# Kernel optimization log

Measured on AMD Instinct MI355X. Metric: run time of the kernel, lower is better.

## Reference

```python
import jax, jax.numpy as jnp
import numpy as np

N_NODES = 50000
N_EDGES = 800000
K = 15          # kernel points
P_DIM = 3
IN_DIM = 32
OUT_DIM = 64
KP_EXTENT = 0.6


def setup_inputs() -> dict:
    key = jax.random.key(0)
    k1, k2, k3, k4, k5, k6 = jax.random.split(key, 6)
    pos = jax.random.normal(k1, (N_NODES, P_DIM), dtype=jnp.float32)
    feat = jax.random.normal(k2, (N_NODES, IN_DIM), dtype=jnp.float32)
    # kernel point layout inside a ball of the given radius (load_kernels stand-in)
    kernel_points = jax.random.normal(k3, (K, P_DIM), dtype=jnp.float32) * 0.5
    kernel_points = kernel_points.at[0].set(0.0)  # fixed center point
    weights = jax.random.normal(k4, (K, IN_DIM, OUT_DIM), dtype=jnp.float32) * (1.0 / np.sqrt(IN_DIM))
    edge_src = jax.random.randint(k5, (N_EDGES,), 0, N_NODES, dtype=jnp.int32)
    edge_dst = jax.random.randint(k6, (N_EDGES,), 0, N_NODES, dtype=jnp.int32)
    return {"pos": pos, "feat": feat, "kernel_points": kernel_points,
            "weights": weights, "edge_src": edge_src, "edge_dst": edge_dst}


def reference(pos, feat, kernel_points, weights, edge_src, edge_dst):
    n_nodes = pos.shape[0]
    # per-edge relative position: src - dst  [E, p]
    y = pos[edge_src] - pos[edge_dst]
    # distance to each kernel point  [E, k]
    diff = y[:, None, :] - kernel_points[None, :, :]
    dist = jnp.sqrt(jnp.sum(diff * diff, axis=-1))
    # linear correlation influence  [E, k]
    m = jax.nn.relu(1.0 - dist / KP_EXTENT)
    # per-edge weighted features  [E, k, in]
    f = feat[edge_src]
    contrib = m[:, :, None] * f[:, None, :]
    # segment-reduce onto destination nodes  [N, k, in]
    weighted_f = jax.ops.segment_sum(contrib, edge_dst, num_segments=n_nodes)
    # per-kernel-point matmul and sum over kernel points  [N, out]
    return jnp.einsum('nki,kio->no', weighted_f, weights)
```

## Files before the change

### kernel.cpp

```cpp
#include <hip/hip_runtime.h>
#include <hip/hip_fp16.h>

#define N_NODES 50000
#define N_EDGES 800000
#define KPTS 15
#define IN_DIM 32
#define OUT_DIM 64
#define KP_EXTENT 0.6f
#define INV_EXT (1.0f / KP_EXTENT)
#define EXT2 (KP_EXTENT * KP_EXTENT)

#define CAP 131072
#define NREP 16
#define SEG_CAP (CAP / NREP)
#define CNT_STRIDE 32
#define K1_BLOCKS (N_EDGES / 256)
#define SUBB 8
#define WPS (SUBB * 4)

#define PCNT_OFF 32768
#define FEATH_OFF (1u << 20)
#define LIST_OFF  (8u << 20)
#define SLOT_OFF  (32u << 20)
#define SCAP_MAX 16

typedef unsigned int uint;
typedef _Float16 f16x8 __attribute__((ext_vector_type(8)));
typedef float f32x4 __attribute__((ext_vector_type(4)));

union FU { uint u[4]; f16x8 h; };

static __device__ __forceinline__ float h2f16(uint u) {
    return __half2float(__ushort_as_half((unsigned short)(u & 0xffffu)));
}
static __device__ __forceinline__ uint pack2(float lo, float hi) {
    return (uint)__half_as_ushort(__float2half_rn(lo))
         | ((uint)__half_as_ushort(__float2half_rn(hi)) << 16);
}

__global__ __launch_bounds__(256) void geom_compact(
    const float* __restrict__ pos,
    const float* __restrict__ feat,
    const float* __restrict__ kp,
    const int*   __restrict__ esrc,
    const int*   __restrict__ edst,
    int*         __restrict__ cnt,
    int*         __restrict__ pcnt,
    uint2*       __restrict__ lists,
    uint*        __restrict__ featH,
    float4*      __restrict__ outz,
    uint*        __restrict__ slots16,
    const int scap)
{
    __shared__ int s_wavecnt[KPTS][4];
    __shared__ int s_woff[KPTS][4];
    __shared__ int s_base[KPTS];

    const int tid  = threadIdx.x;
    const int wv   = tid >> 6;
    const int lane = tid & 63;
    const int rep  = blockIdx.x & (NREP - 1);

    const int e = blockIdx.x * 256 + tid;

    outz[e] = make_float4(0.0f, 0.0f, 0.0f, 0.0f);
    {
        const float2 fv = ((const float2*)feat)[e];
        featH[e] = pack2(fv.x, fv.y);
    }

    const int s = esrc[e];
    const int d = edst[e];

    const float yx = pos[s * 3 + 0] - pos[d * 3 + 0];
    const float yy = pos[s * 3 + 1] - pos[d * 3 + 1];
    const float yz = pos[s * 3 + 2] - pos[d * 3 + 2];

    float d2v[KPTS];
    unsigned act = 0;
    #pragma unroll
    for (int k = 0; k < KPTS; ++k) {
        const float dx = yx - kp[k * 3 + 0];
        const float dy = yy - kp[k * 3 + 1];
        const float dz = yz - kp[k * 3 + 2];
        const float d2 = dx * dx + dy * dy + dz * dz;
        d2v[k] = d2;
        if (d2 < EXT2) act |= (1u << k);
    }

    const int nact = __popc(act);
    int ti = 0;
    if (nact > 0) ti = atomicAdd(pcnt + d, nact);

    unsigned long long kmask[KPTS];
    #pragma unroll
    for (int k = 0; k < KPTS; ++k) {
        kmask[k] = __ballot((act >> k) & 1u);
        if (lane == 0) s_wavecnt[k][wv] = __popcll(kmask[k]);
    }
    __syncthreads();

    if (tid < KPTS) {
        int o0 = 0;
        #pragma unroll
        for (int w = 0; w < 4; ++w) {
            s_woff[tid][w] = o0;
            o0 += s_wavecnt[tid][w];
        }
        s_base[tid] = (o0 > 0)
            ? atomicAdd(&cnt[(tid * NREP + rep) * CNT_STRIDE], o0) : 0;
    }
    __syncthreads();

    const unsigned long long lt = (lane == 63) ? 0x7fffffffffffffffull
                                               : ((1ull << lane) - 1ull);
    #pragma unroll
    for (int k = 0; k < KPTS; ++k) {
        const unsigned long long mask = kmask[k];
        if (mask == 0ull) continue;
        if ((act >> k) & 1u) {
            const int rank = __popcll(mask & lt);
            const int idx  = s_base[k] + s_woff[k][wv] + rank;

            const int t = ti;
            ++ti;
            const unsigned ey = (t < scap)
                ? (unsigned)((d * scap + t) * OUT_DIM)
                : (0x80000000u | (unsigned)d);

            if (idx < SEG_CAP) {
                const float mk = 1.0f - sqrtf(d2v[k]) * INV_EXT;
                const unsigned mh =
                    (unsigned)__half_as_ushort(__float2half(mk));
                lists[(size_t)k * CAP + (size_t)rep * SEG_CAP + idx] =
                    make_uint2(((unsigned)s << 16) | mh, ey);
            } else if (!(ey & 0x80000000u)) {
                uint* row = slots16 + (ey >> 1);
                #pragma unroll
                for (int j = 0; j < OUT_DIM / 2; ++j) row[j] = 0u;
            }
        }
    }
}

__global__ __launch_bounds__(256) void pair_matmul(
    const uint*  __restrict__ featH,
    const float* __restrict__ W,
    const int*   __restrict__ cnt,
    const uint2* __restrict__ lists,
    float*       __restrict__ out,
    uint*        __restrict__ slots16)
{
    const int seg  = blockIdx.x % (KPTS * NREP);
    const int sub  = blockIdx.x / (KPTS * NREP);
    const int k    = seg >> 4;
    const int rep  = seg & (NREP - 1);
    const int wv   = threadIdx.x >> 6;
    const int lane = threadIdx.x & 63;
    const int col  = lane & 15;
    const int grp  = lane >> 4;

    uint bu[4][4];
    const float* __restrict__ Wk = W + k * (IN_DIM * OUT_DIM);
    #pragma unroll
    for (int t = 0; t < 4; ++t) {
        #pragma unroll
        for (int j = 0; j < 4; ++j) {
            const int kk = grp * 8 + 2 * j;
            const float wa = Wk[kk * OUT_DIM + t * 16 + col];
            const float wb = Wk[(kk + 1) * OUT_DIM + t * 16 + col];
            bu[t][j] = pack2(wa, wb);
        }
    }
    #pragma unroll
    for (int t = 0; t < 4; ++t)
        #pragma unroll
        for (int j = 0; j < 4; ++j)
            asm volatile("" : "+v"(bu[t][j]));

    int n = cnt[seg * CNT_STRIDE];
    if (n > SEG_CAP) n = SEG_CAP;
    const uint2* __restrict__ list =
        lists + (size_t)k * CAP + (size_t)rep * SEG_CAP;
    const int nsteps = (n + 15) >> 4;

    const int w = sub * 4 + wv;
    for (int s = w; s < nsteps; s += WPS) {
        const int pi = s * 16 + col;
        const uint2 ent = (pi < n) ? list[pi] : make_uint2(0u, 0xFFFFFFFFu);

        const uint src = ent.x >> 16;
        FU A;
        {
            const uint* __restrict__ fp = featH + src * 16 + grp * 4;
            #pragma unroll
            for (int j = 0; j < 4; ++j) A.u[j] = fp[j];
        }
        const float mym = h2f16(ent.x);

        f32x4 C0 = {0,0,0,0}, C1 = {0,0,0,0}, C2 = {0,0,0,0}, C3 = {0,0,0,0};
        {
            FU b0, b1, b2, b3;
            #pragma unroll
            for (int j = 0; j < 4; ++j) {
                b0.u[j] = bu[0][j]; b1.u[j] = bu[1][j];
                b2.u[j] = bu[2][j]; b3.u[j] = bu[3][j];
            }
            C0 = __builtin_amdgcn_mfma_f32_16x16x32_f16(A.h, b0.h, C0, 0, 0, 0);
            C1 = __builtin_amdgcn_mfma_f32_16x16x32_f16(A.h, b1.h, C1, 0, 0, 0);
            C2 = __builtin_amdgcn_mfma_f32_16x16x32_f16(A.h, b2.h, C2, 0, 0, 0);
            C3 = __builtin_amdgcn_mfma_f32_16x16x32_f16(A.h, b3.h, C3, 0, 0, 0);
        }

        #pragma unroll
        for (int i = 0; i < 4; ++i) {
            const int r = grp * 4 + i;
            const float mr = __shfl(mym, r);
            const uint  er = (uint)__shfl((int)ent.y, r);
            if (er == 0xFFFFFFFFu) continue;
            const float v0 = mr * C0[i];
            const float v1 = mr * C1[i];
            const float v2 = mr * C2[i];
            const float v3 = mr * C3[i];
            if (!(er & 0x80000000u)) {
                __half* __restrict__ sp = (__half*)slots16 + (size_t)er + col;
                sp[0]  = __float2half_rn(v0);
                sp[16] = __float2half_rn(v1);
                sp[32] = __float2half_rn(v2);
                sp[48] = __float2half_rn(v3);
            } else {
                float* __restrict__ op = out + (size_t)(er & 0xffffu) * OUT_DIM + col;
                atomicAdd(op +  0, v0);
                atomicAdd(op + 16, v1);
                atomicAdd(op + 32, v2);
                atomicAdd(op + 48, v3);
            }
        }
    }
}

__global__ __launch_bounds__(256) void node_reduce(
    const int*  __restrict__ pcnt,
    const uint* __restrict__ slots16,
    float*      __restrict__ out,
    const int scap)
{
    const int wv   = threadIdx.x >> 6;
    const int lane = threadIdx.x & 63;
    const int node = blockIdx.x * 8 + wv * 2 + (lane >> 5);
    const int l    = lane & 31;

    const int raw = pcnt[node];
    int deg = raw;
    if (deg > scap) deg = scap;

    const uint* __restrict__ sp =
        slots16 + (size_t)node * ((size_t)scap * 32) + l;

    float a0 = 0.0f, a1 = 0.0f, b0 = 0.0f, b1 = 0.0f;
    int j = 0;
    for (; j + 1 < deg; j += 2) {
        const uint u0 = sp[(size_t)j * 32];
        const uint u1 = sp[(size_t)(j + 1) * 32];
        a0 += h2f16(u0); a1 += h2f16(u0 >> 16);
        b0 += h2f16(u1); b1 += h2f16(u1 >> 16);
    }
    if (j < deg) {
        const uint u0 = sp[(size_t)j * 32];
        a0 += h2f16(u0); a1 += h2f16(u0 >> 16);
    }

    float o0 = a0 + b0;
    float o1 = a1 + b1;
    if (raw > scap) {
        const float2 prev = ((const float2*)out)[(size_t)node * 32 + l];
        o0 += prev.x; o1 += prev.y;
    }
    ((float2*)out)[(size_t)node * 32 + l] = make_float2(o0, o1);
}

extern "C" void kernel_launch(void* const* d_in, const int* in_sizes, int n_in,
                              void* d_out, int out_size, void* d_ws, size_t ws_size,
                              hipStream_t stream)
{
    const float* pos  = (const float*)d_in[0];
    const float* feat = (const float*)d_in[1];
    const float* kp   = (const float*)d_in[2];
    const float* W    = (const float*)d_in[3];
    const int* esrc   = (const int*)d_in[4];
    const int* edst   = (const int*)d_in[5];
    float* out        = (float*)d_out;

    int*   cnt     = (int*)d_ws;
    int*   pcnt    = (int*)((char*)d_ws + PCNT_OFF);
    uint*  featH   = (uint*)((char*)d_ws + FEATH_OFF);
    uint2* lists   = (uint2*)((char*)d_ws + LIST_OFF);
    uint*  slots16 = (uint*)((char*)d_ws + SLOT_OFF);

    const size_t layer_bytes = (size_t)N_NODES * OUT_DIM * 2;
    int scap = 0;
    if (ws_size >= (size_t)SLOT_OFF + layer_bytes) {
        scap = (int)((ws_size - (size_t)SLOT_OFF) / layer_bytes);
        if (scap > SCAP_MAX) scap = SCAP_MAX;
    }

    hipMemsetAsync(d_ws, 0, 262144, stream);

    geom_compact<<<K1_BLOCKS, 256, 0, stream>>>(pos, feat, kp, esrc, edst,
                                                cnt, pcnt, lists, featH,
                                                (float4*)out, slots16, scap);
    pair_matmul<<<SUBB * KPTS * NREP, 256, 0, stream>>>(featH, W, cnt, lists,
                                                        out, slots16);
    if (scap > 0)
        node_reduce<<<N_NODES / 8, 256, 0, stream>>>(pcnt, slots16, out, scap);
}
```

Before: 114.6 us.

## Prepack fp16 weights, prefetch next list entry, fold influence into MFMA input

The fp32-to-fp16 weight packing moves into the first kernel, which writes a packed WH buffer, so pair_matmul blocks load ready-made fp16 pairs instead of converting per block. The pair loop now software-pipelines the next list entry load, and the influence scalar is multiplied into the fp16 feature operand before the MFMA, removing per-row shuffles and multiplies. The number of sub-blocks per segment is halved, giving fewer, longer-running blocks. Scaling in fp16 before the matmul slightly changes rounding, and the smaller grid may reduce parallelism.

After: 113.8 us. Within noise of the previous version (-0.7%).

```diff
diff --git a/kernel.cpp b/kernel.cpp
--- a/kernel.cpp
+++ b/kernel.cpp
@@ -15,10 +15,11 @@
 #define SEG_CAP (CAP / NREP)
 #define CNT_STRIDE 32
 #define K1_BLOCKS (N_EDGES / 256)
-#define SUBB 8
+#define SUBB 4
 #define WPS (SUBB * 4)
 
 #define PCNT_OFF 32768
+#define WH_OFF   262144
 #define FEATH_OFF (1u << 20)
 #define LIST_OFF  (8u << 20)
 #define SLOT_OFF  (32u << 20)
@@ -29,6 +30,7 @@
 typedef float f32x4 __attribute__((ext_vector_type(4)));
 
 union FU { uint u[4]; f16x8 h; };
+union HU { unsigned short us; _Float16 h; };
 
 static __device__ __forceinline__ float h2f16(uint u) {
     return __half2float(__ushort_as_half((unsigned short)(u & 0xffffu)));
@@ -42,12 +44,14 @@
     const float* __restrict__ pos,
     const float* __restrict__ feat,
     const float* __restrict__ kp,
+    const float* __restrict__ W,
     const int*   __restrict__ esrc,
     const int*   __restrict__ edst,
     int*         __restrict__ cnt,
     int*         __restrict__ pcnt,
     uint2*       __restrict__ lists,
     uint*        __restrict__ featH,
+    uint*        __restrict__ WH,
     float4*      __restrict__ outz,
     uint*        __restrict__ slots16,
     const int scap)
@@ -67,6 +71,11 @@
     {
         const float2 fv = ((const float2*)feat)[e];
         featH[e] = pack2(fv.x, fv.y);
+    }
+    if (e < KPTS * (IN_DIM / 2) * OUT_DIM) {
+        const int c  = e & 63;
+        const int f0 = 2 * e - c;
+        WH[e] = pack2(W[f0], W[f0 + 64]);
     }
 
     const int s = esrc[e];
@@ -145,7 +154,7 @@
 
 __global__ __launch_bounds__(256) void pair_matmul(
     const uint*  __restrict__ featH,
-    const float* __restrict__ W,
+    const uint*  __restrict__ WH,
     const int*   __restrict__ cnt,
     const uint2* __restrict__ lists,
     float*       __restrict__ out,
@@ -161,17 +170,12 @@
     const int grp  = lane >> 4;
 
     uint bu[4][4];
-    const float* __restrict__ Wk = W + k * (IN_DIM * OUT_DIM);
-    #pragma unroll
-    for (int t = 0; t < 4; ++t) {
-        #pragma unroll
-        for (int j = 0; j < 4; ++j) {
-            const int kk = grp * 8 + 2 * j;
-            const float wa = Wk[kk * OUT_DIM + t * 16 + col];
-            const float wb = Wk[(kk + 1) * OUT_DIM + t * 16 + col];
-            bu[t][j] = pack2(wa, wb);
-        }
-    }
+    const uint* __restrict__ Whk = WH + k * 1024 + grp * 256 + col;
+    #pragma unroll
+    for (int t = 0; t < 4; ++t)
+        #pragma unroll
+        for (int j = 0; j < 4; ++j)
+            bu[t][j] = Whk[j * 64 + t * 16];
     #pragma unroll
     for (int t = 0; t < 4; ++t)
         #pragma unroll
@@ -184,19 +188,32 @@
         lists + (size_t)k * CAP + (size_t)rep * SEG_CAP;
     const int nsteps = (n + 15) >> 4;
 
-    const int w = sub * 4 + wv;
-    for (int s = w; s < nsteps; s += WPS) {
+    int s = sub * 4 + wv;
+    if (s >= nsteps) return;
+
+    uint2 ent;
+    {
         const int pi = s * 16 + col;
-        const uint2 ent = (pi < n) ? list[pi] : make_uint2(0u, 0xFFFFFFFFu);
-
-        const uint src = ent.x >> 16;
-        FU A;
-        {
-            const uint* __restrict__ fp = featH + src * 16 + grp * 4;
-            #pragma unroll
-            for (int j = 0; j < 4; ++j) A.u[j] = fp[j];
-        }
-        const float mym = h2f16(ent.x);
+        ent = (pi < n) ? list[pi] : make_uint2(0u, 0xFFFFFFFFu);
+    }
+    FU A;
+    {
+        const uint* __restrict__ fp = featH + (ent.x >> 16) * 16 + grp * 4;
+        #pragma unroll
+        for (int j = 0; j < 4; ++j) A.u[j] = fp[j];
+    }
+
+    while (true) {
+        const int s2 = s + WPS;
+        uint2 entN = make_uint2(0u, 0xFFFFFFFFu);
+        if (s2 < nsteps) {
+            const int pi2 = s2 * 16 + col;
+            if (pi2 < n) entN = list[pi2];
+        }
+
+        HU mu; mu.us = (unsigned short)(ent.x & 0xffffu);
+        const f16x8 ms = {mu.h, mu.h, mu.h, mu.h, mu.h, mu.h, mu.h, mu.h};
+        FU As; As.h = A.h * ms;
 
         f32x4 C0 = {0,0,0,0}, C1 = {0,0,0,0}, C2 = {0,0,0,0}, C3 = {0,0,0,0};
         {
@@ -206,36 +223,38 @@
                 b0.u[j] = bu[0][j]; b1.u[j] = bu[1][j];
                 b2.u[j] = bu[2][j]; b3.u[j] = bu[3][j];
             }
-            C0 = __builtin_amdgcn_mfma_f32_16x16x32_f16(A.h, b0.h, C0, 0, 0, 0);
-            C1 = __builtin_amdgcn_mfma_f32_16x16x32_f16(A.h, b1.h, C1, 0, 0, 0);
-            C2 = __builtin_amdgcn_mfma_f32_16x16x32_f16(A.h, b2.h, C2, 0, 0, 0);
-            C3 = __builtin_amdgcn_mfma_f32_16x16x32_f16(A.h, b3.h, C3, 0, 0, 0);
+            C0 = __builtin_amdgcn_mfma_f32_16x16x32_f16(As.h, b0.h, C0, 0, 0, 0);
+            C1 = __builtin_amdgcn_mfma_f32_16x16x32_f16(As.h, b1.h, C1, 0, 0, 0);
+            C2 = __builtin_amdgcn_mfma_f32_16x16x32_f16(As.h, b2.h, C2, 0, 0, 0);
+            C3 = __builtin_amdgcn_mfma_f32_16x16x32_f16(As.h, b3.h, C3, 0, 0, 0);
         }
 
         #pragma unroll
         for (int i = 0; i < 4; ++i) {
             const int r = grp * 4 + i;
-            const float mr = __shfl(mym, r);
-            const uint  er = (uint)__shfl((int)ent.y, r);
+            const uint er = (uint)__shfl((int)ent.y, r);
             if (er == 0xFFFFFFFFu) continue;
-            const float v0 = mr * C0[i];
-            const float v1 = mr * C1[i];
-            const float v2 = mr * C2[i];
-            const float v3 = mr * C3[i];
             if (!(er & 0x80000000u)) {
                 __half* __restrict__ sp = (__half*)slots16 + (size_t)er + col;
-                sp[0]  = __float2half_rn(v0);
-                sp[16] = __float2half_rn(v1);
-                sp[32] = __float2half_rn(v2);
-                sp[48] = __float2half_rn(v3);
+                sp[0]  = __float2half_rn(C0[i]);
+                sp[16] = __float2half_rn(C1[i]);
+                sp[32] = __float2half_rn(C2[i]);
+                sp[48] = __float2half_rn(C3[i]);
             } else {
                 float* __restrict__ op = out + (size_t)(er & 0xffffu) * OUT_DIM + col;
-                atomicAdd(op +  0, v0);
-                atomicAdd(op + 16, v1);
-                atomicAdd(op + 32, v2);
-                atomicAdd(op + 48, v3);
+                atomicAdd(op +  0, C0[i]);
+                atomicAdd(op + 16, C1[i]);
+                atomicAdd(op + 32, C2[i]);
+                atomicAdd(op + 48, C3[i]);
             }
         }
+
+        if (s2 >= nsteps) break;
+        s = s2;
+        ent = entN;
+        const uint* __restrict__ fp = featH + (ent.x >> 16) * 16 + grp * 4;
+        #pragma unroll
+        for (int j = 0; j < 4; ++j) A.u[j] = fp[j];
     }
 }
 
@@ -293,6 +312,7 @@
 
     int*   cnt     = (int*)d_ws;
     int*   pcnt    = (int*)((char*)d_ws + PCNT_OFF);
+    uint*  WH      = (uint*)((char*)d_ws + WH_OFF);
     uint*  featH   = (uint*)((char*)d_ws + FEATH_OFF);
     uint2* lists   = (uint2*)((char*)d_ws + LIST_OFF);
     uint*  slots16 = (uint*)((char*)d_ws + SLOT_OFF);
@@ -306,10 +326,10 @@
 
     hipMemsetAsync(d_ws, 0, 262144, stream);
 
-    geom_compact<<<K1_BLOCKS, 256, 0, stream>>>(pos, feat, kp, esrc, edst,
-                                                cnt, pcnt, lists, featH,
+    geom_compact<<<K1_BLOCKS, 256, 0, stream>>>(pos, feat, kp, W, esrc, edst,
+                                                cnt, pcnt, lists, featH, WH,
                                                 (float4*)out, slots16, scap);
-    pair_matmul<<<SUBB * KPTS * NREP, 256, 0, stream>>>(featH, W, cnt, lists,
+    pair_matmul<<<SUBB * KPTS * NREP, 256, 0, stream>>>(featH, WH, cnt, lists,
                                                         out, slots16);
     if (scap > 0)
         node_reduce<<<N_NODES / 8, 256, 0, stream>>>(pcnt, slots16, out, scap);
```
